# Kernel tuning notes

Measured on AMD Instinct MI355X. Metric: run time of the kernel, lower is better.

Reference implementation:

```python
import jax, jax.numpy as jnp
import numpy as np

N_P = 8192
N_T = 8192
# layer widths from GPNPolicyNet.__init__: (8,8)->(8,8)->(16,16)->(64,64)->(16,16)
DIMS = [(8, 8, 8, 8), (8, 8, 16, 16), (16, 16, 64, 64), (64, 64, 16, 16)]


def setup_inputs() -> dict:
    key = jax.random.key(0)
    ks = iter(jax.random.split(key, 64))
    inp = {
        "p": jax.random.normal(next(ks), (N_P, 8), jnp.float32),
        "t": jax.random.normal(next(ks), (N_T, 8), jnp.float32),
        # sparse-ish 0/1 Petri incidence stored dense (as in the torch module)
        "adj": (jax.random.uniform(next(ks), (N_P, N_T)) < 0.005).astype(jnp.float32),
    }
    for i, (lp_in, lt_in, lp_out, lt_out) in enumerate(DIMS, start=1):
        c = lp_in + lt_in
        sc = 1.0 / np.sqrt(c)
        inp[f"w_p{i}"] = jax.random.uniform(next(ks), (c, lp_out), jnp.float32, -sc, sc)
        inp[f"b_p{i}"] = jnp.zeros((lp_out,), jnp.float32)
        inp[f"w_t{i}"] = jax.random.uniform(next(ks), (c, lt_out), jnp.float32, -sc, sc)
        inp[f"b_t{i}"] = jnp.zeros((lt_out,), jnp.float32)
    sc = 1.0 / np.sqrt(32.0)
    inp["w_ac"] = jax.random.uniform(next(ks), (32, 1), jnp.float32, -sc, sc)
    inp["b_ac"] = jnp.zeros((1,), jnp.float32)
    return inp


def _gcpn(p, t, adj, wp, bp, wt, bt):
    agg_t = adj @ t        # [n_p, lt_in]: places gather from incident transitions
    agg_p = adj.T @ p      # [n_t, lp_in]: transitions gather from incident places
    p_out = jax.nn.relu(jnp.concatenate([p, agg_t], axis=-1) @ wp + bp)
    t_out = jax.nn.relu(jnp.concatenate([agg_p, t], axis=-1) @ wt + bt)
    return p_out, t_out


def reference(p, t, adj,
              w_p1, b_p1, w_t1, b_t1,
              w_p2, b_p2, w_t2, b_t2,
              w_p3, b_p3, w_t3, b_t3,
              w_p4, b_p4, w_t4, b_t4,
              w_ac, b_ac):
    p, t = _gcpn(p, t, adj, w_p1, b_p1, w_t1, b_t1)
    p, t = _gcpn(p, t, adj, w_p2, b_p2, w_t2, b_t2)
    p, t = _gcpn(p, t, adj, w_p3, b_p3, w_t3, b_t3)
    p, t = _gcpn(p, t, adj, w_p4, b_p4, w_t4, b_t4)
    x = jnp.concatenate([adj.T @ p, t], axis=-1)  # [n_t, 32]
    logits = (x @ w_ac + b_ac)[:, 0]              # [n_t]
    return jax.nn.softmax(logits, axis=-1)        # firing distribution over transitions
```

## Files before the change

kernel.cpp:

```cpp
#include <hip/hip_runtime.h>
#include <math.h>

#define N_NODES 8192
#define CAP 128
#define ABLK 2048

struct Params {
    const float4* adj4;
    const float* p; const float* t;
    const float* w_p1; const float* b_p1; const float* w_t1; const float* b_t1;
    const float* w_p2; const float* b_p2; const float* w_t2; const float* b_t2;
    const float* w_p3; const float* b_p3; const float* w_t3; const float* b_t3;
    const float* w_p4; const float* b_p4; const float* w_t4; const float* b_t4;
    const float* w_ac; const float* b_ac;
    int* rowCnt; int* rowIdx; int* colCnt; int* colIdx;
    float* pA; float* pB; float* tA; float* tB; float* logits;
    float4* out4;
};

__global__ __launch_bounds__(256) void phaseA_k(Params P) {
    const int gid = blockIdx.x * 256 + threadIdx.x;
#pragma unroll 1
    for (int k = 0; k < 32; k += 4) {
        float4 w[4];
#pragma unroll
        for (int u = 0; u < 4; ++u)
            w[u] = P.adj4[(size_t)(k + u) * (ABLK * 256) + gid];
#pragma unroll
        for (int u = 0; u < 4; ++u) {
            const int fi = (k + u) * (ABLK * 256) + gid;
            const int r  = fi >> 11;
            const int c4 = fi & 2047;
            if (w[u].x != 0.f || w[u].y != 0.f || w[u].z != 0.f || w[u].w != 0.f) {
                float vals[4] = {w[u].x, w[u].y, w[u].z, w[u].w};
#pragma unroll
                for (int e = 0; e < 4; ++e) {
                    if (vals[e] != 0.f) {
                        int c = c4 * 4 + e;
                        int pr = atomicAdd(&P.rowCnt[r], 1);
                        if (pr < CAP) P.rowIdx[r * CAP + pr] = c;
                        int pc = atomicAdd(&P.colCnt[c], 1);
                        if (pc < CAP) P.colIdx[c * CAP + pc] = r;
                    }
                }
            }
        }
    }
}

template <int CI, int CO, bool RELU, bool TONLY>
__global__ __launch_bounds__(256) void layer_k(Params P,
    const float* __restrict__ pIn, const float* __restrict__ tIn,
    const float* __restrict__ Wp, const float* __restrict__ Bp,
    const float* __restrict__ Wt, const float* __restrict__ Bt,
    float* __restrict__ pOut, float* __restrict__ tOut)
{
    constexpr int C = 2 * CI;
    constexpr int G = 64 / CI;
    __shared__ float sWp[C * CO];
    __shared__ float sWt[C * CO];
    __shared__ float sBp[CO];
    __shared__ float sBt[CO];
    __shared__ float sIn[4][C];

    for (int k = threadIdx.x; k < C * CO; k += 256) { sWp[k] = Wp[k]; sWt[k] = Wt[k]; }
    if (threadIdx.x < CO) { sBp[threadIdx.x] = Bp[threadIdx.x]; sBt[threadIdx.x] = Bt[threadIdx.x]; }
    __syncthreads();

    const int rl = threadIdx.x >> 6, lane = threadIdx.x & 63;
    const int task = blockIdx.x * 4 + rl;
    const int feat = lane & (CI - 1);
    const int grp  = lane / CI;

    const bool tSide = TONLY ? true : (task >= N_NODES);
    const int row = TONLY ? task : (tSide ? task - N_NODES : task);
    const float* self_in = tSide ? tIn : pIn;
    const float* oth_in  = tSide ? pIn : tIn;
    const int* cnt  = tSide ? P.colCnt : P.rowCnt;
    const int* idxl = tSide ? P.colIdx : P.rowIdx;
    const float* sW  = tSide ? sWt : sWp;
    const float* sBv = tSide ? sBt : sBp;

    int m = cnt[row];
    if (m > CAP) m = CAP;
    const int* __restrict__ lst = idxl + row * CAP;

    const int len = (m + G - 1) / G;
    const int s0 = grp * len;
    const int s1 = min(s0 + len, m);
    float acc = 0.f;
    int s = s0;
    for (; s + 8 <= s1; s += 8) {
        int j0 = lst[s],     j1 = lst[s + 1], j2 = lst[s + 2], j3 = lst[s + 3];
        int j4 = lst[s + 4], j5 = lst[s + 5], j6 = lst[s + 6], j7 = lst[s + 7];
        float a0 = oth_in[j0 * CI + feat];
        float a1 = oth_in[j1 * CI + feat];
        float a2 = oth_in[j2 * CI + feat];
        float a3 = oth_in[j3 * CI + feat];
        float a4 = oth_in[j4 * CI + feat];
        float a5 = oth_in[j5 * CI + feat];
        float a6 = oth_in[j6 * CI + feat];
        float a7 = oth_in[j7 * CI + feat];
        acc += ((a0 + a1) + (a2 + a3)) + ((a4 + a5) + (a6 + a7));
    }
    for (; s + 4 <= s1; s += 4) {
        int j0 = lst[s], j1 = lst[s + 1], j2 = lst[s + 2], j3 = lst[s + 3];
        float a0 = oth_in[j0 * CI + feat];
        float a1 = oth_in[j1 * CI + feat];
        float a2 = oth_in[j2 * CI + feat];
        float a3 = oth_in[j3 * CI + feat];
        acc += (a0 + a1) + (a2 + a3);
    }
    for (; s < s1; ++s) acc += oth_in[lst[s] * CI + feat];
#pragma unroll
    for (int off = 32; off >= CI; off >>= 1) acc += __shfl_down(acc, off);

    if (lane < CI) {
        const int aggOff  = tSide ? 0 : CI;
        const int selfOff = tSide ? CI : 0;
        sIn[rl][aggOff + lane]  = acc;
        sIn[rl][selfOff + lane] = self_in[row * CI + lane];
    }
    __syncthreads();
    if (lane < CO) {
        float o = sBv[lane];
#pragma unroll
        for (int k = 0; k < C; ++k) o += sIn[rl][k] * sW[k * CO + lane];
        if (RELU) o = fmaxf(o, 0.f);
        (tSide ? tOut : pOut)[row * CO + lane] = o;
    }
}

__global__ __launch_bounds__(1024) void softmax_k(const float4* __restrict__ logits4,
                                                  float4* __restrict__ out4) {
    __shared__ float red[1024];
    float4 a = logits4[threadIdx.x];
    float4 b = logits4[threadIdx.x + 1024];
    float mx = fmaxf(fmaxf(fmaxf(a.x, a.y), fmaxf(a.z, a.w)),
                     fmaxf(fmaxf(b.x, b.y), fmaxf(b.z, b.w)));
    red[threadIdx.x] = mx;
    __syncthreads();
    for (int s = 512; s > 0; s >>= 1) {
        if (threadIdx.x < s) red[threadIdx.x] = fmaxf(red[threadIdx.x], red[threadIdx.x + s]);
        __syncthreads();
    }
    mx = red[0];
    __syncthreads();
    a.x = __expf(a.x - mx); a.y = __expf(a.y - mx);
    a.z = __expf(a.z - mx); a.w = __expf(a.w - mx);
    b.x = __expf(b.x - mx); b.y = __expf(b.y - mx);
    b.z = __expf(b.z - mx); b.w = __expf(b.w - mx);
    float sum = ((a.x + a.y) + (a.z + a.w)) + ((b.x + b.y) + (b.z + b.w));
    red[threadIdx.x] = sum;
    __syncthreads();
    for (int s = 512; s > 0; s >>= 1) {
        if (threadIdx.x < s) red[threadIdx.x] += red[threadIdx.x + s];
        __syncthreads();
    }
    float inv = 1.f / red[0];
    a.x *= inv; a.y *= inv; a.z *= inv; a.w *= inv;
    b.x *= inv; b.y *= inv; b.z *= inv; b.w *= inv;
    out4[threadIdx.x] = a;
    out4[threadIdx.x + 1024] = b;
}

extern "C" void kernel_launch(void* const* d_in, const int* in_sizes, int n_in,
                              void* d_out, int out_size, void* d_ws, size_t ws_size,
                              hipStream_t stream) {
    char* ws = (char*)d_ws;
    Params prm;
    prm.adj4 = (const float4*)d_in[2];
    prm.p    = (const float*)d_in[0];
    prm.t    = (const float*)d_in[1];
    prm.w_p1 = (const float*)d_in[3];  prm.b_p1 = (const float*)d_in[4];
    prm.w_t1 = (const float*)d_in[5];  prm.b_t1 = (const float*)d_in[6];
    prm.w_p2 = (const float*)d_in[7];  prm.b_p2 = (const float*)d_in[8];
    prm.w_t2 = (const float*)d_in[9];  prm.b_t2 = (const float*)d_in[10];
    prm.w_p3 = (const float*)d_in[11]; prm.b_p3 = (const float*)d_in[12];
    prm.w_t3 = (const float*)d_in[13]; prm.b_t3 = (const float*)d_in[14];
    prm.w_p4 = (const float*)d_in[15]; prm.b_p4 = (const float*)d_in[16];
    prm.w_t4 = (const float*)d_in[17]; prm.b_t4 = (const float*)d_in[18];
    prm.w_ac = (const float*)d_in[19]; prm.b_ac = (const float*)d_in[20];

    const size_t MB = 1024 * 1024;
    prm.rowCnt = (int*)(ws);
    prm.colCnt = (int*)(ws + 32768);
    prm.rowIdx = (int*)(ws + 1 * MB);
    prm.colIdx = (int*)(ws + 5 * MB);
    prm.pA     = (float*)(ws + 9 * MB);
    prm.pB     = (float*)(ws + 11 * MB);
    prm.tA     = (float*)(ws + 13 * MB);
    prm.tB     = (float*)(ws + 15 * MB);
    prm.logits = (float*)(ws + 17 * MB);
    prm.out4   = (float4*)d_out;

    hipMemsetAsync(ws, 0, 65536, stream);

    phaseA_k<<<ABLK, 256, 0, stream>>>(prm);

    layer_k<8, 8, true, false><<<N_NODES / 2, 256, 0, stream>>>(
        prm, prm.p, prm.t, prm.w_p1, prm.b_p1, prm.w_t1, prm.b_t1, prm.pA, prm.tA);
    layer_k<8, 16, true, false><<<N_NODES / 2, 256, 0, stream>>>(
        prm, prm.pA, prm.tA, prm.w_p2, prm.b_p2, prm.w_t2, prm.b_t2, prm.pB, prm.tB);
    layer_k<16, 64, true, false><<<N_NODES / 2, 256, 0, stream>>>(
        prm, prm.pB, prm.tB, prm.w_p3, prm.b_p3, prm.w_t3, prm.b_t3, prm.pA, prm.tA);
    layer_k<64, 16, true, false><<<N_NODES / 2, 256, 0, stream>>>(
        prm, prm.pA, prm.tA, prm.w_p4, prm.b_p4, prm.w_t4, prm.b_t4, prm.pB, prm.tB);
    layer_k<16, 1, false, true><<<N_NODES / 4, 256, 0, stream>>>(
        prm, prm.pB, prm.tB, prm.w_ac, prm.b_ac, prm.w_ac, prm.b_ac, prm.logits, prm.logits);

    softmax_k<<<1, 1024, 0, stream>>>((const float4*)prm.logits, prm.out4);
}
```

Before: 493.6 us.

## Build adjacency via tiled bitmasks, fuse list build into layer 1, pair rows

Replaces global atomic-append adjacency extraction with a tiled pass that sets row/column bitmasks in shared memory, then a per-row popcount/prefix-scan kernel that builds sorted neighbor lists and runs layer 1 in the same kernel. This removes contended global atomics and the memset, and gives deterministic list order. Later layers process two rows per wavefront to raise memory-level parallelism. The cost is extra bitmask write/read traffic (16 MB) and an extra pass.

```diff
diff --git a/kernel.cpp b/kernel.cpp
--- a/kernel.cpp
+++ b/kernel.cpp
@@ -3,7 +3,7 @@
 
 #define N_NODES 8192
 #define CAP 128
-#define ABLK 2048
+#define WPR 256
 
 struct Params {
     const float4* adj4;
@@ -13,43 +13,150 @@
     const float* w_p3; const float* b_p3; const float* w_t3; const float* b_t3;
     const float* w_p4; const float* b_p4; const float* w_t4; const float* b_t4;
     const float* w_ac; const float* b_ac;
+    unsigned* rowBits; unsigned* colBits;
     int* rowCnt; int* rowIdx; int* colCnt; int* colIdx;
     float* pA; float* pB; float* tA; float* tB; float* logits;
     float4* out4;
 };
 
-__global__ __launch_bounds__(256) void phaseA_k(Params P) {
-    const int gid = blockIdx.x * 256 + threadIdx.x;
-#pragma unroll 1
-    for (int k = 0; k < 32; k += 4) {
-        float4 w[4];
-#pragma unroll
-        for (int u = 0; u < 4; ++u)
-            w[u] = P.adj4[(size_t)(k + u) * (ABLK * 256) + gid];
-#pragma unroll
-        for (int u = 0; u < 4; ++u) {
-            const int fi = (k + u) * (ABLK * 256) + gid;
-            const int r  = fi >> 11;
-            const int c4 = fi & 2047;
-            if (w[u].x != 0.f || w[u].y != 0.f || w[u].z != 0.f || w[u].w != 0.f) {
-                float vals[4] = {w[u].x, w[u].y, w[u].z, w[u].w};
-#pragma unroll
-                for (int e = 0; e < 4; ++e) {
-                    if (vals[e] != 0.f) {
-                        int c = c4 * 4 + e;
-                        int pr = atomicAdd(&P.rowCnt[r], 1);
-                        if (pr < CAP) P.rowIdx[r * CAP + pr] = c;
-                        int pc = atomicAdd(&P.colCnt[c], 1);
-                        if (pc < CAP) P.colIdx[c * CAP + pc] = r;
-                    }
+__global__ __launch_bounds__(256) void build_bits(Params P) {
+    __shared__ unsigned rb[128 * 4];
+    __shared__ unsigned cb[128 * 4];
+    const int tid = threadIdx.x;
+    rb[tid] = 0; rb[tid + 256] = 0;
+    cb[tid] = 0; cb[tid + 256] = 0;
+    __syncthreads();
+
+    const int tileR = blockIdx.x >> 6;
+    const int tileC = blockIdx.x & 63;
+    const int R0 = tileR * 128;
+    const int C0 = tileC * 128;
+
+    float4 v[16];
+#pragma unroll
+    for (int k = 0; k < 16; ++k) {
+        int fi = k * 256 + tid;
+        int r  = fi >> 5;
+        int c4 = fi & 31;
+        v[k] = P.adj4[(size_t)(R0 + r) * 2048 + (C0 >> 2) + c4];
+    }
+#pragma unroll
+    for (int k = 0; k < 16; ++k) {
+        int fi = k * 256 + tid;
+        int r  = fi >> 5;
+        int cb4 = (fi & 31) * 4;
+        float vals[4] = {v[k].x, v[k].y, v[k].z, v[k].w};
+        if (vals[0] != 0.f || vals[1] != 0.f || vals[2] != 0.f || vals[3] != 0.f) {
+#pragma unroll
+            for (int e = 0; e < 4; ++e) {
+                if (vals[e] != 0.f) {
+                    int c = cb4 + e;
+                    atomicOr(&rb[r * 4 + (c >> 5)], 1u << (c & 31));
+                    atomicOr(&cb[c * 4 + (r >> 5)], 1u << (r & 31));
                 }
             }
         }
     }
+    __syncthreads();
+    if (tid < 128) {
+        uint4 q = make_uint4(rb[tid * 4], rb[tid * 4 + 1], rb[tid * 4 + 2], rb[tid * 4 + 3]);
+        *(uint4*)(P.rowBits + (size_t)(R0 + tid) * WPR + tileC * 4) = q;
+    } else {
+        int c = tid - 128;
+        uint4 q = make_uint4(cb[c * 4], cb[c * 4 + 1], cb[c * 4 + 2], cb[c * 4 + 3]);
+        *(uint4*)(P.colBits + (size_t)(C0 + c) * WPR + tileR * 4) = q;
+    }
+}
+
+__global__ __launch_bounds__(256) void lists_layer1_k(Params P) {
+    __shared__ int  slst[4][CAP];
+    __shared__ float sWp[16 * 8];
+    __shared__ float sWt[16 * 8];
+    __shared__ float sBp[8];
+    __shared__ float sBt[8];
+    __shared__ float sIn[4][16];
+
+    for (int k = threadIdx.x; k < 128; k += 256) { sWp[k] = P.w_p1[k]; sWt[k] = P.w_t1[k]; }
+    if (threadIdx.x < 8) { sBp[threadIdx.x] = P.b_p1[threadIdx.x]; sBt[threadIdx.x] = P.b_t1[threadIdx.x]; }
+
+    const int rl = threadIdx.x >> 6, lane = threadIdx.x & 63;
+    const int id = blockIdx.x * 4 + rl;
+    const bool tSide = id >= N_NODES;
+    const int n = tSide ? id - N_NODES : id;
+    const unsigned* bits = (tSide ? P.colBits : P.rowBits) + (size_t)n * WPR;
+    int* cnt = tSide ? P.colCnt : P.rowCnt;
+    int* lst = (tSide ? P.colIdx : P.rowIdx) + n * CAP;
+
+    uint4 w4 = ((const uint4*)bits)[lane];
+    int pc = __popc(w4.x) + __popc(w4.y) + __popc(w4.z) + __popc(w4.w);
+    int incl = pc;
+    for (int d = 1; d < 64; d <<= 1) {
+        int nv = __shfl_up(incl, d);
+        if (lane >= d) incl += nv;
+    }
+    int off = incl - pc;
+    int total = __shfl(incl, 63);
+    unsigned wds[4] = {w4.x, w4.y, w4.z, w4.w};
+    const int base = lane * 128;
+#pragma unroll
+    for (int w = 0; w < 4; ++w) {
+        unsigned word = wds[w];
+        while (word) {
+            int b = __ffs(word) - 1;
+            word &= word - 1;
+            if (off < CAP) {
+                int idx = base + w * 32 + b;
+                lst[off] = idx;
+                slst[rl][off] = idx;
+            }
+            ++off;
+        }
+    }
+    int m = total > CAP ? CAP : total;
+    if (lane == 0) cnt[n] = m;
+    __syncthreads();
+
+    const float* oth_in  = tSide ? P.p : P.t;
+    const float* self_in = tSide ? P.t : P.p;
+    const int feat = lane & 7;
+    const int grp  = lane >> 3;
+    const int len = (m + 7) >> 3;
+    int s = grp * len;
+    const int s1 = min(s + len, m);
+    float acc = 0.f;
+    for (; s + 8 <= s1; s += 8) {
+        int j0 = slst[rl][s],     j1 = slst[rl][s + 1], j2 = slst[rl][s + 2], j3 = slst[rl][s + 3];
+        int j4 = slst[rl][s + 4], j5 = slst[rl][s + 5], j6 = slst[rl][s + 6], j7 = slst[rl][s + 7];
+        float a0 = oth_in[j0 * 8 + feat], a1 = oth_in[j1 * 8 + feat];
+        float a2 = oth_in[j2 * 8 + feat], a3 = oth_in[j3 * 8 + feat];
+        float a4 = oth_in[j4 * 8 + feat], a5 = oth_in[j5 * 8 + feat];
+        float a6 = oth_in[j6 * 8 + feat], a7 = oth_in[j7 * 8 + feat];
+        acc += ((a0 + a1) + (a2 + a3)) + ((a4 + a5) + (a6 + a7));
+    }
+    for (; s < s1; ++s) acc += oth_in[slst[rl][s] * 8 + feat];
+#pragma unroll
+    for (int o = 32; o >= 8; o >>= 1) acc += __shfl_down(acc, o);
+
+    if (lane < 8) {
+        const int aggOff  = tSide ? 0 : 8;
+        const int selfOff = tSide ? 8 : 0;
+        sIn[rl][aggOff + lane]  = acc;
+        sIn[rl][selfOff + lane] = self_in[n * 8 + lane];
+    }
+    __syncthreads();
+    if (lane < 8) {
+        const float* sW  = tSide ? sWt : sWp;
+        const float* sBv = tSide ? sBt : sBp;
+        float o = sBv[lane];
+#pragma unroll
+        for (int k = 0; k < 16; ++k) o += sIn[rl][k] * sW[k * 8 + lane];
+        o = fmaxf(o, 0.f);
+        (tSide ? P.tA : P.pA)[n * 8 + lane] = o;
+    }
 }
 
 template <int CI, int CO, bool RELU, bool TONLY>
-__global__ __launch_bounds__(256) void layer_k(Params P,
+__global__ __launch_bounds__(256) void layer2_k(Params P,
     const float* __restrict__ pIn, const float* __restrict__ tIn,
     const float* __restrict__ Wp, const float* __restrict__ Bp,
     const float* __restrict__ Wt, const float* __restrict__ Bt,
@@ -61,73 +168,114 @@
     __shared__ float sWt[C * CO];
     __shared__ float sBp[CO];
     __shared__ float sBt[CO];
-    __shared__ float sIn[4][C];
+    __shared__ float sIn[8][C];
 
     for (int k = threadIdx.x; k < C * CO; k += 256) { sWp[k] = Wp[k]; sWt[k] = Wt[k]; }
     if (threadIdx.x < CO) { sBp[threadIdx.x] = Bp[threadIdx.x]; sBt[threadIdx.x] = Bt[threadIdx.x]; }
     __syncthreads();
 
     const int rl = threadIdx.x >> 6, lane = threadIdx.x & 63;
-    const int task = blockIdx.x * 4 + rl;
     const int feat = lane & (CI - 1);
     const int grp  = lane / CI;
-
-    const bool tSide = TONLY ? true : (task >= N_NODES);
-    const int row = TONLY ? task : (tSide ? task - N_NODES : task);
-    const float* self_in = tSide ? tIn : pIn;
-    const float* oth_in  = tSide ? pIn : tIn;
-    const int* cnt  = tSide ? P.colCnt : P.rowCnt;
-    const int* idxl = tSide ? P.colIdx : P.rowIdx;
-    const float* sW  = tSide ? sWt : sWp;
-    const float* sBv = tSide ? sBt : sBp;
-
-    int m = cnt[row];
-    if (m > CAP) m = CAP;
-    const int* __restrict__ lst = idxl + row * CAP;
-
-    const int len = (m + G - 1) / G;
-    const int s0 = grp * len;
-    const int s1 = min(s0 + len, m);
-    float acc = 0.f;
-    int s = s0;
-    for (; s + 8 <= s1; s += 8) {
-        int j0 = lst[s],     j1 = lst[s + 1], j2 = lst[s + 2], j3 = lst[s + 3];
-        int j4 = lst[s + 4], j5 = lst[s + 5], j6 = lst[s + 6], j7 = lst[s + 7];
-        float a0 = oth_in[j0 * CI + feat];
-        float a1 = oth_in[j1 * CI + feat];
-        float a2 = oth_in[j2 * CI + feat];
-        float a3 = oth_in[j3 * CI + feat];
-        float a4 = oth_in[j4 * CI + feat];
-        float a5 = oth_in[j5 * CI + feat];
-        float a6 = oth_in[j6 * CI + feat];
-        float a7 = oth_in[j7 * CI + feat];
-        acc += ((a0 + a1) + (a2 + a3)) + ((a4 + a5) + (a6 + a7));
-    }
-    for (; s + 4 <= s1; s += 4) {
-        int j0 = lst[s], j1 = lst[s + 1], j2 = lst[s + 2], j3 = lst[s + 3];
-        float a0 = oth_in[j0 * CI + feat];
-        float a1 = oth_in[j1 * CI + feat];
-        float a2 = oth_in[j2 * CI + feat];
-        float a3 = oth_in[j3 * CI + feat];
-        acc += (a0 + a1) + (a2 + a3);
-    }
-    for (; s < s1; ++s) acc += oth_in[lst[s] * CI + feat];
-#pragma unroll
-    for (int off = 32; off >= CI; off >>= 1) acc += __shfl_down(acc, off);
+    const int taskA = (blockIdx.x * 4 + rl) * 2;
+    const int taskB = taskA + 1;
+
+    const bool tsA = TONLY ? true : (taskA >= N_NODES);
+    const int rowA = TONLY ? taskA : (tsA ? taskA - N_NODES : taskA);
+    const float* othA = tsA ? pIn : tIn;
+    int mA = (tsA ? P.colCnt : P.rowCnt)[rowA];
+    if (mA > CAP) mA = CAP;
+    const int* __restrict__ lstA = (tsA ? P.colIdx : P.rowIdx) + rowA * CAP;
+    const int lenA = (mA + G - 1) / G;
+    int sA = grp * lenA;
+    const int s1A = min(sA + lenA, mA);
+    const bool tsB = TONLY ? true : (taskB >= N_NODES);
+    const int rowB = TONLY ? taskB : (tsB ? taskB - N_NODES : taskB);
+    const float* othB = tsB ? pIn : tIn;
+    int mB = (tsB ? P.colCnt : P.rowCnt)[rowB];
+    if (mB > CAP) mB = CAP;
+    const int* __restrict__ lstB = (tsB ? P.colIdx : P.rowIdx) + rowB * CAP;
+    const int lenB = (mB + G - 1) / G;
+    int sB = grp * lenB;
+    const int s1B = min(sB + lenB, mB);
+
+    float accA = 0.f, accB = 0.f;
+    while (sA + 8 <= s1A && sB + 8 <= s1B) {
+        int a0 = lstA[sA],     a1 = lstA[sA + 1], a2 = lstA[sA + 2], a3 = lstA[sA + 3];
+        int a4 = lstA[sA + 4], a5 = lstA[sA + 5], a6 = lstA[sA + 6], a7 = lstA[sA + 7];
+        int b0 = lstB[sB],     b1 = lstB[sB + 1], b2 = lstB[sB + 2], b3 = lstB[sB + 3];
+        int b4 = lstB[sB + 4], b5 = lstB[sB + 5], b6 = lstB[sB + 6], b7 = lstB[sB + 7];
+        float fa0 = othA[a0 * CI + feat], fa1 = othA[a1 * CI + feat];
+        float fa2 = othA[a2 * CI + feat], fa3 = othA[a3 * CI + feat];
+        float fa4 = othA[a4 * CI + feat], fa5 = othA[a5 * CI + feat];
+        float fa6 = othA[a6 * CI + feat], fa7 = othA[a7 * CI + feat];
+        float fb0 = othB[b0 * CI + feat], fb1 = othB[b1 * CI + feat];
+        float fb2 = othB[b2 * CI + feat], fb3 = othB[b3 * CI + feat];
+        float fb4 = othB[b4 * CI + feat], fb5 = othB[b5 * CI + feat];
+        float fb6 = othB[b6 * CI + feat], fb7 = othB[b7 * CI + feat];
+        accA += ((fa0 + fa1) + (fa2 + fa3)) + ((fa4 + fa5) + (fa6 + fa7));
+        accB += ((fb0 + fb1) + (fb2 + fb3)) + ((fb4 + fb5) + (fb6 + fb7));
+        sA += 8; sB += 8;
+    }
+    for (; sA + 8 <= s1A; sA += 8) {
+        int a0 = lstA[sA],     a1 = lstA[sA + 1], a2 = lstA[sA + 2], a3 = lstA[sA + 3];
+        int a4 = lstA[sA + 4], a5 = lstA[sA + 5], a6 = lstA[sA + 6], a7 = lstA[sA + 7];
+        float fa0 = othA[a0 * CI + feat], fa1 = othA[a1 * CI + feat];
+        float fa2 = othA[a2 * CI + feat], fa3 = othA[a3 * CI + feat];
+        float fa4 = othA[a4 * CI + feat], fa5 = othA[a5 * CI + feat];
+        float fa6 = othA[a6 * CI + feat], fa7 = othA[a7 * CI + feat];
+        accA += ((fa0 + fa1) + (fa2 + fa3)) + ((fa4 + fa5) + (fa6 + fa7));
+    }
+    for (; sB + 8 <= s1B; sB += 8) {
+        int b0 = lstB[sB],     b1 = lstB[sB + 1], b2 = lstB[sB + 2], b3 = lstB[sB + 3];
+        int b4 = lstB[sB + 4], b5 = lstB[sB + 5], b6 = lstB[sB + 6], b7 = lstB[sB + 7];
+        float fb0 = othB[b0 * CI + feat], fb1 = othB[b1 * CI + feat];
+        float fb2 = othB[b2 * CI + feat], fb3 = othB[b3 * CI + feat];
+        float fb4 = othB[b4 * CI + feat], fb5 = othB[b5 * CI + feat];
+        float fb6 = othB[b6 * CI + feat], fb7 = othB[b7 * CI + feat];
+        accB += ((fb0 + fb1) + (fb2 + fb3)) + ((fb4 + fb5) + (fb6 + fb7));
+    }
+    for (; sA + 4 <= s1A; sA += 4) {
+        int a0 = lstA[sA], a1 = lstA[sA + 1], a2 = lstA[sA + 2], a3 = lstA[sA + 3];
+        accA += (othA[a0 * CI + feat] + othA[a1 * CI + feat])
+              + (othA[a2 * CI + feat] + othA[a3 * CI + feat]);
+    }
+    for (; sB + 4 <= s1B; sB += 4) {
+        int b0 = lstB[sB], b1 = lstB[sB + 1], b2 = lstB[sB + 2], b3 = lstB[sB + 3];
+        accB += (othB[b0 * CI + feat] + othB[b1 * CI + feat])
+              + (othB[b2 * CI + feat] + othB[b3 * CI + feat]);
+    }
+    for (; sA < s1A; ++sA) accA += othA[lstA[sA] * CI + feat];
+    for (; sB < s1B; ++sB) accB += othB[lstB[sB] * CI + feat];
+
+#pragma unroll
+    for (int o = 32; o >= CI; o >>= 1) {
+        accA += __shfl_down(accA, o);
+        accB += __shfl_down(accB, o);
+    }
 
     if (lane < CI) {
-        const int aggOff  = tSide ? 0 : CI;
-        const int selfOff = tSide ? CI : 0;
-        sIn[rl][aggOff + lane]  = acc;
-        sIn[rl][selfOff + lane] = self_in[row * CI + lane];
+        const float* selfA = tsA ? tIn : pIn;
+        const float* selfB = tsB ? tIn : pIn;
+        sIn[rl * 2][(tsA ? 0 : CI) + lane]     = accA;
+        sIn[rl * 2][(tsA ? CI : 0) + lane]     = selfA[rowA * CI + lane];
+        sIn[rl * 2 + 1][(tsB ? 0 : CI) + lane] = accB;
+        sIn[rl * 2 + 1][(tsB ? CI : 0) + lane] = selfB[rowB * CI + lane];
     }
     __syncthreads();
     if (lane < CO) {
-        float o = sBv[lane];
-#pragma unroll
-        for (int k = 0; k < C; ++k) o += sIn[rl][k] * sW[k * CO + lane];
-        if (RELU) o = fmaxf(o, 0.f);
-        (tSide ? tOut : pOut)[row * CO + lane] = o;
+        const float* sWA = tsA ? sWt : sWp;
+        const float* sWB = tsB ? sWt : sWp;
+        float oA = (tsA ? sBt : sBp)[lane];
+        float oB = (tsB ? sBt : sBp)[lane];
+#pragma unroll
+        for (int k = 0; k < C; ++k) {
+            oA += sIn[rl * 2][k]     * sWA[k * CO + lane];
+            oB += sIn[rl * 2 + 1][k] * sWB[k * CO + lane];
+        }
+        if (RELU) { oA = fmaxf(oA, 0.f); oB = fmaxf(oB, 0.f); }
+        (tsA ? tOut : pOut)[rowA * CO + lane] = oA;
+        (tsB ? tOut : pOut)[rowB * CO + lane] = oB;
     }
 }
 
@@ -183,31 +331,28 @@
     prm.w_ac = (const float*)d_in[19]; prm.b_ac = (const float*)d_in[20];
 
     const size_t MB = 1024 * 1024;
-    prm.rowCnt = (int*)(ws);
-    prm.colCnt = (int*)(ws + 32768);
-    prm.rowIdx = (int*)(ws + 1 * MB);
-    prm.colIdx = (int*)(ws + 5 * MB);
-    prm.pA     = (float*)(ws + 9 * MB);
-    prm.pB     = (float*)(ws + 11 * MB);
-    prm.tA     = (float*)(ws + 13 * MB);
-    prm.tB     = (float*)(ws + 15 * MB);
-    prm.logits = (float*)(ws + 17 * MB);
-    prm.out4   = (float4*)d_out;
-
-    hipMemsetAsync(ws, 0, 65536, stream);
-
-    phaseA_k<<<ABLK, 256, 0, stream>>>(prm);
-
-    layer_k<8, 8, true, false><<<N_NODES / 2, 256, 0, stream>>>(
-        prm, prm.p, prm.t, prm.w_p1, prm.b_p1, prm.w_t1, prm.b_t1, prm.pA, prm.tA);
-    layer_k<8, 16, true, false><<<N_NODES / 2, 256, 0, stream>>>(
+    prm.rowCnt  = (int*)(ws);
+    prm.colCnt  = (int*)(ws + 32768);
+    prm.rowIdx  = (int*)(ws + 1 * MB);
+    prm.colIdx  = (int*)(ws + 5 * MB);
+    prm.rowBits = (unsigned*)(ws + 9 * MB);
+    prm.colBits = (unsigned*)(ws + 17 * MB);
+    prm.pA      = (float*)(ws + 25 * MB);
+    prm.pB      = (float*)(ws + 27 * MB);
+    prm.tA      = (float*)(ws + 29 * MB);
+    prm.tB      = (float*)(ws + 31 * MB);
+    prm.logits  = (float*)(ws + 33 * MB);
+    prm.out4    = (float4*)d_out;
+
+    build_bits<<<4096, 256, 0, stream>>>(prm);
+    lists_layer1_k<<<4096, 256, 0, stream>>>(prm);
+    layer2_k<8, 16, true, false><<<2048, 256, 0, stream>>>(
         prm, prm.pA, prm.tA, prm.w_p2, prm.b_p2, prm.w_t2, prm.b_t2, prm.pB, prm.tB);
-    layer_k<16, 64, true, false><<<N_NODES / 2, 256, 0, stream>>>(
+    layer2_k<16, 64, true, false><<<2048, 256, 0, stream>>>(
         prm, prm.pB, prm.tB, prm.w_p3, prm.b_p3, prm.w_t3, prm.b_t3, prm.pA, prm.tA);
-    layer_k<64, 16, true, false><<<N_NODES / 2, 256, 0, stream>>>(
+    layer2_k<64, 16, true, false><<<2048, 256, 0, stream>>>(
         prm, prm.pA, prm.tA, prm.w_p4, prm.b_p4, prm.w_t4, prm.b_t4, prm.pB, prm.tB);
-    layer_k<16, 1, false, true><<<N_NODES / 4, 256, 0, stream>>>(
+    layer2_k<16, 1, false, true><<<1024, 256, 0, stream>>>(
         prm, prm.pB, prm.tB, prm.w_ac, prm.b_ac, prm.w_ac, prm.b_ac, prm.logits, prm.logits);
-
     softmax_k<<<1, 1024, 0, stream>>>((const float4*)prm.logits, prm.out4);
 }
```

Result: faster. 472.7 us (-4.2%).
